# Kernel tuning notes

Hardware: AMD Instinct MI355X
Metric: run time of the kernel (lower is better)

## Reference

```python
import jax, jax.numpy as jnp
import numpy as np

PARAM_BOUNDS = {'R': (1e-4, 0.2), 'C': (1e5, 1e8), 'A_eff': (0.0, 0.2), 'hvac_gain': (1.0, 2e4)}
PARAM_INIT = {'R': 0.007, 'C': 3.5e6, 'A_eff': 0.01, 'hvac_gain': 450.0}
DELTA_T = 900.0  # seconds per step (from args.delta_t)
COOLING_SIGN = -1.0  # mode == 'cool'


def _raw_init(name):
    lo, hi = PARAM_BOUNDS[name]
    p = (PARAM_INIT[name] - lo) / (hi - lo)
    return np.float32(np.log(p / (1.0 - p)))  # logit


def _bounded(raw, lo, hi):
    return lo + (hi - lo) * jax.nn.sigmoid(raw)


def setup_inputs() -> dict:
    key = jax.random.key(0)
    B, S = 8192, 4096
    input_vec = jax.random.normal(key, (B, S, 4), dtype=jnp.float32)
    return {
        'input_vec': input_vec,
        'raw_R': jnp.asarray(_raw_init('R')),
        'raw_C': jnp.asarray(_raw_init('C')),
        'raw_A_eff': jnp.asarray(_raw_init('A_eff')),
        'raw_hvac_gain': jnp.asarray(_raw_init('hvac_gain')),
    }


def reference(input_vec, raw_R, raw_C, raw_A_eff, raw_hvac_gain):
    R = _bounded(raw_R, *PARAM_BOUNDS['R'])
    C = _bounded(raw_C, *PARAM_BOUNDS['C'])
    A_eff = _bounded(raw_A_eff, *PARAM_BOUNDS['A_eff'])
    g = _bounded(raw_hvac_gain, *PARAM_BOUNDS['hvac_gain'])

    t_in = input_vec[:, :, 0]   # (B, S)
    t_out = input_vec[:, :, 1]
    hvac_u = input_vec[:, :, 2]
    solar = input_vec[:, :, 3]

    def step(t_prev, x):
        to, u, so = x
        heat = (to - t_prev) / R
        hvac = COOLING_SIGN * g * u
        sol = A_eff * so
        t_next = t_prev + DELTA_T * (heat + hvac + sol) / C
        return t_next, t_next

    t0 = t_in[:, 0]  # initial indoor temperature, (B,)
    xs = (t_out.T, hvac_u.T, solar.T)  # time-major (S, B)
    _, preds = jax.lax.scan(step, t0, xs)  # preds: (S, B)
    return jnp.transpose(preds)[..., None]  # (B, S, 1)
```

## Files before the change

kernel.cpp:

```cpp
#include <hip/hip_runtime.h>
#include <math.h>


#define SLEN 4096
#define THREADS 256
#define PER 16

__global__ __launch_bounds__(THREADS) void rc_scan_kernel(
    const float* __restrict__ in,
    const float* __restrict__ rawR,
    const float* __restrict__ rawC,
    const float* __restrict__ rawA,
    const float* __restrict__ rawG,
    float* __restrict__ out)
{
    __shared__ float sm_m[THREADS];
    __shared__ float sm_d[THREADS];

    const int row = blockIdx.x;
    const int tid = threadIdx.x;

    const float sR = 1.0f / (1.0f + expf(-rawR[0]));
    const float sC = 1.0f / (1.0f + expf(-rawC[0]));
    const float sA = 1.0f / (1.0f + expf(-rawA[0]));
    const float sG = 1.0f / (1.0f + expf(-rawG[0]));
    const float R = 0.0001f + (0.2f - 0.0001f) * sR;
    const float C = 100000.0f + (100000000.0f - 100000.0f) * sC;
    const float A = 0.2f * sA;
    const float g = 1.0f + (20000.0f - 1.0f) * sG;

    const float k     = 900.0f / C;
    const float kinvR = k / R;
    const float a     = 1.0f - kinvR;
    const float kg    = k * g;
    const float kA    = k * A;

    const float4* rowp = (const float4*)(in + (size_t)row * (size_t)SLEN * 4);

    const float t0 = rowp[0].x;

    float c[PER];
#pragma unroll
    for (int j = 0; j < PER; ++j) {
        float4 v = rowp[tid * PER + j];
        c[j] = kinvR * v.y - kg * v.z + kA * v.w;
    }

    float d = 0.0f;
#pragma unroll
    for (int j = 0; j < PER; ++j) d = a * d + c[j];
    const float a2 = a * a, a4 = a2 * a2, a8 = a4 * a4;
    const float m16 = a8 * a8;

    float cm = m16, cd = d;
    sm_m[tid] = cm;
    sm_d[tid] = cd;
    __syncthreads();
    for (int off = 1; off < THREADS; off <<= 1) {
        float pm = 1.0f, pd = 0.0f;
        const bool has = (tid >= off);
        if (has) { pm = sm_m[tid - off]; pd = sm_d[tid - off]; }
        __syncthreads();
        if (has) { cd = cm * pd + cd; cm = pm * cm; }
        sm_m[tid] = cm;
        sm_d[tid] = cd;
        __syncthreads();
    }

    float t;
    if (tid == 0) t = t0;
    else          t = sm_m[tid - 1] * t0 + sm_d[tid - 1];

    float os[PER];
#pragma unroll
    for (int j = 0; j < PER; ++j) {
        t = a * t + c[j];
        os[j] = t;
    }

    float4* outp = (float4*)(out + (size_t)row * SLEN + (size_t)tid * PER);
#pragma unroll
    for (int q = 0; q < PER / 4; ++q) {
        outp[q] = make_float4(os[4 * q + 0], os[4 * q + 1],
                              os[4 * q + 2], os[4 * q + 3]);
    }
}

extern "C" void kernel_launch(void* const* d_in, const int* in_sizes, int n_in,
                              void* d_out, int out_size, void* d_ws, size_t ws_size,
                              hipStream_t stream) {
    const float* in   = (const float*)d_in[0];
    const float* rawR = (const float*)d_in[1];
    const float* rawC = (const float*)d_in[2];
    const float* rawA = (const float*)d_in[3];
    const float* rawG = (const float*)d_in[4];
    float* out = (float*)d_out;

    const int B = in_sizes[0] / (SLEN * 4);
    rc_scan_kernel<<<dim3(B), dim3(THREADS), 0, stream>>>(
        in, rawR, rawC, rawA, rawG, out);
}
```

Baseline: 741.6 us.

## Stage inputs and outputs through padded shared memory for coalesced global access

Loads the per-step float4 inputs with a thread-strided pattern so consecutive threads read consecutive elements, computes the forcing term into a padded shared buffer, then has each thread read back its contiguous chunk for the blocked scan. Outputs are written back into the same padded buffer and stored as coalesced float4 rows. This targets the strided, uncoalesced global loads and stores of the old per-thread-chunk layout, at the cost of extra LDS traffic, more barriers and a larger shared allocation that may reduce occupancy. Explicit fmaf calls are also added.

```diff
diff --git a/kernel.cpp b/kernel.cpp
--- a/kernel.cpp
+++ b/kernel.cpp
@@ -5,6 +5,7 @@
 #define SLEN 4096
 #define THREADS 256
 #define PER 16
+#define PAD_IDX(s) ((((s) >> 4) * 17) + ((s) & 15))
 
 __global__ __launch_bounds__(THREADS) void rc_scan_kernel(
     const float* __restrict__ in,
@@ -14,6 +15,7 @@
     const float* __restrict__ rawG,
     float* __restrict__ out)
 {
+    __shared__ float sm_c[256 * 17];
     __shared__ float sm_m[THREADS];
     __shared__ float sm_d[THREADS];
 
@@ -39,16 +41,21 @@
 
     const float t0 = rowp[0].x;
 
+#pragma unroll
+    for (int q = 0; q < PER; ++q) {
+        const int s = tid + THREADS * q;
+        float4 v = rowp[s];
+        sm_c[PAD_IDX(s)] = kinvR * v.y - kg * v.z + kA * v.w;
+    }
+    __syncthreads();
+
     float c[PER];
 #pragma unroll
-    for (int j = 0; j < PER; ++j) {
-        float4 v = rowp[tid * PER + j];
-        c[j] = kinvR * v.y - kg * v.z + kA * v.w;
-    }
+    for (int j = 0; j < PER; ++j) c[j] = sm_c[tid * 17 + j];
 
     float d = 0.0f;
 #pragma unroll
-    for (int j = 0; j < PER; ++j) d = a * d + c[j];
+    for (int j = 0; j < PER; ++j) d = fmaf(a, d, c[j]);
     const float a2 = a * a, a4 = a2 * a2, a8 = a4 * a4;
     const float m16 = a8 * a8;
 
@@ -61,7 +68,7 @@
         const bool has = (tid >= off);
         if (has) { pm = sm_m[tid - off]; pd = sm_d[tid - off]; }
         __syncthreads();
-        if (has) { cd = cm * pd + cd; cm = pm * cm; }
+        if (has) { cd = fmaf(cm, pd, cd); cm = pm * cm; }
         sm_m[tid] = cm;
         sm_d[tid] = cd;
         __syncthreads();
@@ -69,20 +76,25 @@
 
     float t;
     if (tid == 0) t = t0;
-    else          t = sm_m[tid - 1] * t0 + sm_d[tid - 1];
+    else          t = fmaf(sm_m[tid - 1], t0, sm_d[tid - 1]);
 
-    float os[PER];
 #pragma unroll
     for (int j = 0; j < PER; ++j) {
-        t = a * t + c[j];
-        os[j] = t;
+        t = fmaf(a, t, c[j]);
+        sm_c[tid * 17 + j] = t;
     }
+    __syncthreads();
 
-    float4* outp = (float4*)(out + (size_t)row * SLEN + (size_t)tid * PER);
+    float* orow = out + (size_t)row * SLEN;
 #pragma unroll
-    for (int q = 0; q < PER / 4; ++q) {
-        outp[q] = make_float4(os[4 * q + 0], os[4 * q + 1],
-                              os[4 * q + 2], os[4 * q + 3]);
+    for (int q = 0; q < 4; ++q) {
+        const int s0 = q * 1024 + 4 * tid;
+        float4 v;
+        v.x = sm_c[PAD_IDX(s0 + 0)];
+        v.y = sm_c[PAD_IDX(s0 + 1)];
+        v.z = sm_c[PAD_IDX(s0 + 2)];
+        v.w = sm_c[PAD_IDX(s0 + 3)];
+        *(float4*)(orow + s0) = v;
     }
 }
 
```

After: 719.4 us. 1.03x faster.
